# Performance work log

Measured on AMD Instinct MI355X. Metric: run time of the kernel, lower is better.

The kernel has to match this reference:

```python
import jax, jax.numpy as jnp
import numpy as np

B, T, D = 8, 4096, 256
K = 8192  # codebook_size


def setup_inputs() -> dict:
    key = jax.random.key(0)
    k1, k2 = jax.random.split(key)
    h = jax.random.normal(k1, (B, T, D), dtype=jnp.float32)
    # nn.init.uniform_(codebook.weight, -1.0, 1.0)
    codebook = jax.random.uniform(k2, (K, D), dtype=jnp.float32, minval=-1.0, maxval=1.0)
    return {"h": h, "codebook": codebook}


def reference(h, codebook):
    b, t, d = h.shape
    flat = h.reshape(-1, d)                              # [N, D]
    x2 = jnp.sum(flat * flat, axis=1, keepdims=True)     # [N, 1]
    c2 = jnp.sum(codebook * codebook, axis=1)[None, :]   # [1, K]
    xc = flat @ codebook.T                               # [N, K]
    dist = x2 + c2 - 2.0 * xc                            # [N, K]
    idx_flat = jnp.argmin(dist, axis=1)                  # [N] int
    q_flat = codebook[idx_flat]                          # gather [N, D]
    q = q_flat.reshape(b, t, d)
    idx = idx_flat.reshape(b, t)
    # straight-through estimator
    q_ste = h + jax.lax.stop_gradient(q - h)
    return q_ste, idx
```

## Files before the change

### kernel.cpp

```cpp
#include <hip/hip_runtime.h>

typedef short short8 __attribute__((ext_vector_type(8)));
typedef float f32x4 __attribute__((ext_vector_type(4)));

#define DIMS   256
#define KCODES 8192
#define NTOK   32768
#define BM     128
#define BN     128
#define NTILES 64
#define MARGIN 0.75f
#define CAP    6144

__device__ __forceinline__ unsigned short f2bf(float f) {
    unsigned u = __builtin_bit_cast(unsigned, f);
    unsigned r = (u + 0x7FFFu + ((u >> 16) & 1u)) >> 16;
    return (unsigned short)r;
}
__device__ __forceinline__ unsigned fenc(float f) {
    unsigned u = __builtin_bit_cast(unsigned, f);
    return ((int)u >= 0) ? (u | 0x80000000u) : ~u;
}
__device__ __forceinline__ float fdec(unsigned e) {
    unsigned u = (e & 0x80000000u) ? (e ^ 0x80000000u) : ~e;
    return __builtin_bit_cast(float, u);
}
template <int CTRL>
__device__ __forceinline__ float ror_min(float x) {
    int xi = __builtin_bit_cast(int, x);
    int r  = __builtin_amdgcn_update_dpp(xi, xi, CTRL, 0xF, 0xF, false);
    return fminf(x, __builtin_bit_cast(float, r));
}
__device__ __forceinline__ float rowmin16(float x) {
    x = ror_min<0x121>(x);
    x = ror_min<0x122>(x);
    x = ror_min<0x124>(x);
    x = ror_min<0x128>(x);
    return x;
}

__global__ __launch_bounds__(256) void prep_kernel(const float* __restrict__ cb,
                                                   float* __restrict__ c2,
                                                   unsigned short* __restrict__ cbbf,
                                                   int do_conv) {
    int row  = blockIdx.x * 4 + (threadIdx.x >> 6);
    int lane = threadIdx.x & 63;
    float4 v = *(const float4*)(cb + (size_t)row * DIMS + (size_t)lane * 4);
    if (do_conv) {
        ushort4 s;
        s.x = f2bf(v.x); s.y = f2bf(v.y); s.z = f2bf(v.z); s.w = f2bf(v.w);
        *(ushort4*)(cbbf + (size_t)row * DIMS + (size_t)lane * 4) = s;
    }
    float s = v.x * v.x + v.y * v.y + v.z * v.z + v.w * v.w;
#pragma unroll
    for (int off = 32; off > 0; off >>= 1) s += __shfl_down(s, off);
    if (lane == 0) c2[row] = s;
}

template <bool WSBF>
__global__ __launch_bounds__(512, 2) void vq_main(const float* __restrict__ h,
                                                  const float* __restrict__ cb,
                                                  const unsigned short* __restrict__ cbbf,
                                                  const float* __restrict__ c2g,
                                                  float* __restrict__ out_q,
                                                  float* __restrict__ out_idx) {
    __shared__ __align__(16) unsigned short Bs[2][BN * DIMS];
    __shared__ unsigned mrun[BM];
    __shared__ unsigned list[CAP];
    __shared__ int cnt;

    const int tid  = threadIdx.x;
    const int lane = tid & 63;
    const int wave = tid >> 6;
    const int l15  = lane & 15;
    const int quad = lane >> 4;
    const int wm   = wave >> 2;
    const int wn   = wave & 3;
    const int tokBase = blockIdx.x * BM;

    if (tid < BM) mrun[tid] = 0xFFFFFFFFu;
    if (tid == 0) cnt = 0;

    const int srow = tid >> 5;
    const int sc8  = tid & 31;
    const int sswz = sc8 ^ (srow & 7);

    short8 g[8];
    auto stage_load = [&](int t) {
#pragma unroll
        for (int n = 0; n < 8; n++) {
            const size_t off = (size_t)(t * BN + srow + n * 16) * DIMS + sc8 * 8;
            if constexpr (WSBF) {
                g[n] = *(const short8*)(cbbf + off);
            } else {
                float4 v0 = *(const float4*)(cb + off);
                float4 v1 = *(const float4*)(cb + off + 4);
                short8 s;
                s[0] = f2bf(v0.x); s[1] = f2bf(v0.y); s[2] = f2bf(v0.z); s[3] = f2bf(v0.w);
                s[4] = f2bf(v1.x); s[5] = f2bf(v1.y); s[6] = f2bf(v1.z); s[7] = f2bf(v1.w);
                g[n] = s;
            }
        }
    };
    auto stage_write = [&](int buf) {
        unsigned short* dst = &Bs[buf][srow * DIMS + sswz * 8];
#pragma unroll
        for (int n = 0; n < 8; n++)
            *(short8*)(dst + n * 16 * DIMS) = g[n];
    };

    stage_load(0);

    short8 afr[4][8];
#pragma unroll
    for (int i = 0; i < 4; i++) {
        const float* base = h + (size_t)(tokBase + wm * 64 + i * 16 + l15) * DIMS + quad * 8;
#pragma unroll
        for (int kk = 0; kk < 8; kk++) {
            float4 v0 = *(const float4*)(base + kk * 32);
            float4 v1 = *(const float4*)(base + kk * 32 + 4);
            short8 s;
            s[0] = f2bf(v0.x); s[1] = f2bf(v0.y); s[2] = f2bf(v0.z); s[3] = f2bf(v0.w);
            s[4] = f2bf(v1.x); s[5] = f2bf(v1.y); s[6] = f2bf(v1.z); s[7] = f2bf(v1.w);
            afr[i][kk] = s;
        }
    }

    stage_write(0);

    const int bswz = l15 & 7;
    const int bq   = (quad ^ (bswz & 3)) << 3;
    const int bx4  = (bswz & 4) << 3;

#pragma unroll 1
    for (int it = 0; it <= NTILES; ++it) {
        const int t = (it == NTILES) ? 0 : it;
        __syncthreads();
        const int cur = it & 1;
        if (it < NTILES) stage_load((it + 1 == NTILES) ? 0 : it + 1);

        const float cc0 = c2g[t * BN + wn * 32 + l15];
        const float cc1 = c2g[t * BN + wn * 32 + 16 + l15];

        const unsigned short* bp = &Bs[cur][(wn * 32 + l15) * DIMS + bq];

        f32x4 acc[4][2];
#pragma unroll
        for (int i = 0; i < 4; i++) { acc[i][0] = (f32x4){0,0,0,0}; acc[i][1] = (f32x4){0,0,0,0}; }

        __builtin_amdgcn_s_setprio(1);
#pragma unroll
        for (int kk = 0; kk < 8; kk++) {
            const int off = (kk * 32) ^ bx4;
            short8 b0 = *(const short8*)(bp + off);
            short8 b1 = *(const short8*)(bp + off + 16 * DIMS);
#pragma unroll
            for (int i = 0; i < 4; i++) {
                acc[i][0] = __builtin_amdgcn_mfma_f32_16x16x32_bf16(afr[i][kk], b0, acc[i][0], 0, 0, 0);
                acc[i][1] = __builtin_amdgcn_mfma_f32_16x16x32_bf16(afr[i][kk], b1, acc[i][1], 0, 0, 0);
            }
        }
        __builtin_amdgcn_s_setprio(0);

        const int code0 = t * BN + wn * 32 + l15;
#pragma unroll
        for (int i = 0; i < 4; i++) {
            const int tokb = wm * 64 + i * 16 + quad * 4;
            float thr0 = 0, thr1 = 0, thr2 = 0, thr3 = 0;
            if (it > 0) {
                thr0 = fdec(mrun[tokb + 0]) + MARGIN;
                thr1 = fdec(mrun[tokb + 1]) + MARGIN;
                thr2 = fdec(mrun[tokb + 2]) + MARGIN;
                thr3 = fdec(mrun[tokb + 3]) + MARGIN;
            }
            float vm0 = 3.4e38f, vm1 = 3.4e38f, vm2 = 3.4e38f, vm3 = 3.4e38f;
#pragma unroll
            for (int j = 0; j < 2; j++) {
                const float cc = j ? cc1 : cc0;
                const int code = j ? code0 + 16 : code0;
                float s0 = fmaf(-2.f, acc[i][j][0], cc);
                float s1 = fmaf(-2.f, acc[i][j][1], cc);
                float s2 = fmaf(-2.f, acc[i][j][2], cc);
                float s3 = fmaf(-2.f, acc[i][j][3], cc);
                vm0 = fminf(vm0, s0); vm1 = fminf(vm1, s1);
                vm2 = fminf(vm2, s2); vm3 = fminf(vm3, s3);
                if (it > 0) {
                    if (s0 <= thr0) { int p = atomicAdd(&cnt, 1); if (p < CAP) list[p] = (unsigned)(((tokb + 0) << 13) | code); }
                    if (s1 <= thr1) { int p = atomicAdd(&cnt, 1); if (p < CAP) list[p] = (unsigned)(((tokb + 1) << 13) | code); }
                    if (s2 <= thr2) { int p = atomicAdd(&cnt, 1); if (p < CAP) list[p] = (unsigned)(((tokb + 2) << 13) | code); }
                    if (s3 <= thr3) { int p = atomicAdd(&cnt, 1); if (p < CAP) list[p] = (unsigned)(((tokb + 3) << 13) | code); }
                }
            }
            if (it < NTILES) {
                vm0 = rowmin16(vm0); vm1 = rowmin16(vm1);
                vm2 = rowmin16(vm2); vm3 = rowmin16(vm3);
                if (l15 == 0) {
                    atomicMin(&mrun[tokb + 0], fenc(vm0));
                    atomicMin(&mrun[tokb + 1], fenc(vm1));
                    atomicMin(&mrun[tokb + 2], fenc(vm2));
                    atomicMin(&mrun[tokb + 3], fenc(vm3));
                }
            }
        }
        if (it < NTILES) stage_write(cur ^ 1);
    }
    __syncthreads();

    unsigned long long* best64 = (unsigned long long*)&Bs[0][0];
    if (tid < BM) best64[tid] = ~0ULL;
    __syncthreads();

    int n = cnt; if (n > CAP) n = CAP;
    for (int p = wave; p < n; p += 8) {
        unsigned e = list[p];
        int tok = (int)(e >> 13), code = (int)(e & 8191);
        float4 hv = *(const float4*)(h + (size_t)(tokBase + tok) * DIMS + lane * 4);
        float4 cv = *(const float4*)(cb + (size_t)code * DIMS + lane * 4);
        float d = hv.x * cv.x + hv.y * cv.y + hv.z * cv.z + hv.w * cv.w;
#pragma unroll
        for (int m = 1; m < 64; m <<= 1) d += __shfl_xor(d, m);
        float s = c2g[code] - 2.f * d;
        if (lane == 0)
            atomicMin(&best64[tok], ((unsigned long long)fenc(s) << 32) | (unsigned)code);
    }
    __syncthreads();

    if (tid < BM)
        out_idx[tokBase + tid] = (float)(unsigned)(best64[tid] & 0xFFFFFFFFULL);
#pragma unroll
    for (int e = tid; e < BM * (DIMS / 4); e += 512) {
        int r = e >> 6, c4 = e & 63;
        int idx = (int)(unsigned)(best64[r] & 0xFFFFFFFFULL);
        float4 v = *(const float4*)(cb + (size_t)idx * DIMS + c4 * 4);
        *(float4*)(out_q + (size_t)(tokBase + r) * DIMS + c4 * 4) = v;
    }
}

extern "C" void kernel_launch(void* const* d_in, const int* in_sizes, int n_in,
                              void* d_out, int out_size, void* d_ws, size_t ws_size,
                              hipStream_t stream) {
    const float* h  = (const float*)d_in[0];
    const float* cb = (const float*)d_in[1];
    float* out_q   = (float*)d_out;
    float* out_idx = (float*)d_out + (size_t)NTOK * DIMS;

    float* c2 = (float*)d_ws;
    unsigned short* cbbf = (unsigned short*)((char*)d_ws + 32768);
    const size_t needed = 32768 + (size_t)KCODES * DIMS * 2;
    const int wsbf = (ws_size >= needed) ? 1 : 0;

    prep_kernel<<<KCODES / 4, 256, 0, stream>>>(cb, c2, cbbf, wsbf);
    if (wsbf)
        vq_main<true><<<NTOK / BM, 512, 0, stream>>>(h, cb, cbbf, c2, out_q, out_idx);
    else
        vq_main<false><<<NTOK / BM, 512, 0, stream>>>(h, cb, (const unsigned short*)nullptr, c2, out_q, out_idx);
}
```

Measured before the change: 436.9 us.

## Swap MFMA operands so each lane owns one token, simplifying min reduction

Swaps the A/B operands of the bf16 MFMA so that each lane's accumulator holds four codes for a single token instead of four tokens for a single code. The per-token min then becomes a local fmin tree plus two cross-quad shuffles, replacing four DPP row reductions and four LDS atomicMin calls per row group with one. The threshold and c2 loads are hoisted and vectorised, and the next stage's shared-memory write is moved ahead of the epilogue. The candidate-list logic is otherwise unchanged, but the earlier stage_write changes when the double-buffered stores land relative to the epilogue's LDS atomics.

```diff
diff --git a/kernel.cpp b/kernel.cpp
--- a/kernel.cpp
+++ b/kernel.cpp
@@ -24,19 +24,6 @@
 __device__ __forceinline__ float fdec(unsigned e) {
     unsigned u = (e & 0x80000000u) ? (e ^ 0x80000000u) : ~e;
     return __builtin_bit_cast(float, u);
-}
-template <int CTRL>
-__device__ __forceinline__ float ror_min(float x) {
-    int xi = __builtin_bit_cast(int, x);
-    int r  = __builtin_amdgcn_update_dpp(xi, xi, CTRL, 0xF, 0xF, false);
-    return fminf(x, __builtin_bit_cast(float, r));
-}
-__device__ __forceinline__ float rowmin16(float x) {
-    x = ror_min<0x121>(x);
-    x = ror_min<0x122>(x);
-    x = ror_min<0x124>(x);
-    x = ror_min<0x128>(x);
-    return x;
 }
 
 __global__ __launch_bounds__(256) void prep_kernel(const float* __restrict__ cb,
@@ -139,8 +126,16 @@
         const int cur = it & 1;
         if (it < NTILES) stage_load((it + 1 == NTILES) ? 0 : it + 1);
 
-        const float cc0 = c2g[t * BN + wn * 32 + l15];
-        const float cc1 = c2g[t * BN + wn * 32 + 16 + l15];
+        float thr[4];
+        const bool haveThr = (it > 0);
+        if (haveThr) {
+#pragma unroll
+            for (int i = 0; i < 4; i++)
+                thr[i] = fdec(mrun[wm * 64 + i * 16 + l15]) + MARGIN;
+        }
+        const int cbase = t * BN + wn * 32;
+        const float4 cc0 = *(const float4*)(c2g + cbase + quad * 4);
+        const float4 cc1 = *(const float4*)(c2g + cbase + 16 + quad * 4);
 
         const unsigned short* bp = &Bs[cur][(wn * 32 + l15) * DIMS + bq];
 
@@ -156,53 +151,46 @@
             short8 b1 = *(const short8*)(bp + off + 16 * DIMS);
 #pragma unroll
             for (int i = 0; i < 4; i++) {
-                acc[i][0] = __builtin_amdgcn_mfma_f32_16x16x32_bf16(afr[i][kk], b0, acc[i][0], 0, 0, 0);
-                acc[i][1] = __builtin_amdgcn_mfma_f32_16x16x32_bf16(afr[i][kk], b1, acc[i][1], 0, 0, 0);
+                acc[i][0] = __builtin_amdgcn_mfma_f32_16x16x32_bf16(b0, afr[i][kk], acc[i][0], 0, 0, 0);
+                acc[i][1] = __builtin_amdgcn_mfma_f32_16x16x32_bf16(b1, afr[i][kk], acc[i][1], 0, 0, 0);
             }
         }
         __builtin_amdgcn_s_setprio(0);
 
-        const int code0 = t * BN + wn * 32 + l15;
+        if (it < NTILES) stage_write(cur ^ 1);
+
+        const int code00 = cbase + quad * 4;
 #pragma unroll
         for (int i = 0; i < 4; i++) {
-            const int tokb = wm * 64 + i * 16 + quad * 4;
-            float thr0 = 0, thr1 = 0, thr2 = 0, thr3 = 0;
-            if (it > 0) {
-                thr0 = fdec(mrun[tokb + 0]) + MARGIN;
-                thr1 = fdec(mrun[tokb + 1]) + MARGIN;
-                thr2 = fdec(mrun[tokb + 2]) + MARGIN;
-                thr3 = fdec(mrun[tokb + 3]) + MARGIN;
-            }
-            float vm0 = 3.4e38f, vm1 = 3.4e38f, vm2 = 3.4e38f, vm3 = 3.4e38f;
-#pragma unroll
-            for (int j = 0; j < 2; j++) {
-                const float cc = j ? cc1 : cc0;
-                const int code = j ? code0 + 16 : code0;
-                float s0 = fmaf(-2.f, acc[i][j][0], cc);
-                float s1 = fmaf(-2.f, acc[i][j][1], cc);
-                float s2 = fmaf(-2.f, acc[i][j][2], cc);
-                float s3 = fmaf(-2.f, acc[i][j][3], cc);
-                vm0 = fminf(vm0, s0); vm1 = fminf(vm1, s1);
-                vm2 = fminf(vm2, s2); vm3 = fminf(vm3, s3);
-                if (it > 0) {
-                    if (s0 <= thr0) { int p = atomicAdd(&cnt, 1); if (p < CAP) list[p] = (unsigned)(((tokb + 0) << 13) | code); }
-                    if (s1 <= thr1) { int p = atomicAdd(&cnt, 1); if (p < CAP) list[p] = (unsigned)(((tokb + 1) << 13) | code); }
-                    if (s2 <= thr2) { int p = atomicAdd(&cnt, 1); if (p < CAP) list[p] = (unsigned)(((tokb + 2) << 13) | code); }
-                    if (s3 <= thr3) { int p = atomicAdd(&cnt, 1); if (p < CAP) list[p] = (unsigned)(((tokb + 3) << 13) | code); }
-                }
+            const int tok = wm * 64 + i * 16 + l15;
+            float s0 = fmaf(-2.f, acc[i][0][0], cc0.x);
+            float s1 = fmaf(-2.f, acc[i][0][1], cc0.y);
+            float s2 = fmaf(-2.f, acc[i][0][2], cc0.z);
+            float s3 = fmaf(-2.f, acc[i][0][3], cc0.w);
+            float s4 = fmaf(-2.f, acc[i][1][0], cc1.x);
+            float s5 = fmaf(-2.f, acc[i][1][1], cc1.y);
+            float s6 = fmaf(-2.f, acc[i][1][2], cc1.z);
+            float s7 = fmaf(-2.f, acc[i][1][3], cc1.w);
+            float vm = fminf(fminf(fminf(s0, s1), fminf(s2, s3)),
+                             fminf(fminf(s4, s5), fminf(s6, s7)));
+            if (haveThr) {
+                const float th = thr[i];
+                const unsigned tk = (unsigned)(tok << 13);
+                if (s0 <= th) { int p = atomicAdd(&cnt, 1); if (p < CAP) list[p] = tk | (unsigned)(code00 + 0); }
+                if (s1 <= th) { int p = atomicAdd(&cnt, 1); if (p < CAP) list[p] = tk | (unsigned)(code00 + 1); }
+                if (s2 <= th) { int p = atomicAdd(&cnt, 1); if (p < CAP) list[p] = tk | (unsigned)(code00 + 2); }
+                if (s3 <= th) { int p = atomicAdd(&cnt, 1); if (p < CAP) list[p] = tk | (unsigned)(code00 + 3); }
+                if (s4 <= th) { int p = atomicAdd(&cnt, 1); if (p < CAP) list[p] = tk | (unsigned)(code00 + 16); }
+                if (s5 <= th) { int p = atomicAdd(&cnt, 1); if (p < CAP) list[p] = tk | (unsigned)(code00 + 17); }
+                if (s6 <= th) { int p = atomicAdd(&cnt, 1); if (p < CAP) list[p] = tk | (unsigned)(code00 + 18); }
+                if (s7 <= th) { int p = atomicAdd(&cnt, 1); if (p < CAP) list[p] = tk | (unsigned)(code00 + 19); }
             }
             if (it < NTILES) {
-                vm0 = rowmin16(vm0); vm1 = rowmin16(vm1);
-                vm2 = rowmin16(vm2); vm3 = rowmin16(vm3);
-                if (l15 == 0) {
-                    atomicMin(&mrun[tokb + 0], fenc(vm0));
-                    atomicMin(&mrun[tokb + 1], fenc(vm1));
-                    atomicMin(&mrun[tokb + 2], fenc(vm2));
-                    atomicMin(&mrun[tokb + 3], fenc(vm3));
-                }
-            }
-        }
-        if (it < NTILES) stage_write(cur ^ 1);
+                vm = fminf(vm, __shfl_xor(vm, 16));
+                vm = fminf(vm, __shfl_xor(vm, 32));
+                if (quad == 0) atomicMin(&mrun[tok], fenc(vm));
+            }
+        }
     }
     __syncthreads();
 
```

Measured after the change: 397.1 us. -9.1%, faster.
